# Kernel tuning notes

Hardware: AMD Instinct MI355X
Metric: run time of the kernel (lower is better)

Reference implementation:

```python
import jax, jax.numpy as jnp
import numpy as np

N_NODES = 50000
N_EDGES = 800000
DIM = 256
DEPTH = 4
N_REL = 4
EPS = 1e-5


def setup_inputs() -> dict:
    key = jax.random.key(0)
    ks = jax.random.split(key, 8)
    scale = 1.0 / np.sqrt(DIM)
    return {
        "node_embedding": jax.random.normal(ks[0], (N_NODES, DIM), jnp.float32),
        "weights": jax.random.normal(ks[1], (DEPTH, N_REL, DIM, DIM), jnp.float32) * scale,
        "roots": jax.random.normal(ks[2], (DEPTH, DIM, DIM), jnp.float32) * scale,
        "biases": jax.random.normal(ks[3], (DEPTH, DIM), jnp.float32) * 0.01,
        "ln_gamma": jnp.ones((DEPTH, DIM), jnp.float32),
        "ln_beta": jnp.zeros((DEPTH, DIM), jnp.float32),
        "edge_index": jax.random.randint(ks[4], (2, N_EDGES), 0, N_NODES, jnp.int32),
        "edge_type": jax.random.randint(ks[5], (N_EDGES,), 0, N_REL, jnp.int32),
    }


def _rgcn_layer(X, W, root, bias, gamma, beta, src, dst, etype, inv_deg):
    # RGCNConv with aggr='mean': per-relation transform, then per-relation mean
    # over incoming edges at the target node, summed across relations.
    h = jnp.einsum('ni,rio->rno', X, W)            # [R, N, D]
    msg = h[etype, src] * inv_deg[:, None]         # [E, D] gather + per-relation 1/deg
    agg = jax.ops.segment_sum(msg, dst, num_segments=X.shape[0])  # [N, D]
    out = agg + X @ root + bias
    # LayerNorm
    mu = jnp.mean(out, axis=-1, keepdims=True)
    var = jnp.mean(jnp.square(out - mu), axis=-1, keepdims=True)
    out = (out - mu) * jax.lax.rsqrt(var + EPS) * gamma + beta
    out = jax.nn.elu(out)
    return out + X  # residual connection (dropout p=0 -> identity)


def reference(node_embedding, weights, roots, biases, ln_gamma, ln_beta, edge_index, edge_type):
    src, dst = edge_index[0], edge_index[1]
    # per-(node, relation) in-degree for the relation-wise mean aggregation
    cnt = jnp.zeros((node_embedding.shape[0], N_REL), node_embedding.dtype)
    cnt = cnt.at[dst, edge_type].add(1.0)
    inv_deg = 1.0 / jnp.maximum(cnt[dst, edge_type], 1.0)  # [E]
    X = node_embedding
    for l in range(DEPTH):
        X = _rgcn_layer(X, weights[l], roots[l], biases[l], ln_gamma[l], ln_beta[l],
                        src, dst, edge_type, inv_deg)
    return X
```

## Files before the change

kernel.cpp:

```cpp
#include <hip/hip_runtime.h>
#include <hip/hip_bf16.h>
#include <stdint.h>

#define NN 50000
#define NE 800000
#define DD 256
#define NL 4
#define NRL 4
#define KT 1280
#define KA 1024

typedef float f32x4 __attribute__((ext_vector_type(4)));
typedef __bf16 bf16x8 __attribute__((ext_vector_type(8)));
typedef __bf16 bf16x4 __attribute__((ext_vector_type(4)));
typedef unsigned short u16x4 __attribute__((ext_vector_type(4)));

static __device__ __forceinline__ unsigned short f2bf(float f) {
  __bf16 h = (__bf16)f;
  return __builtin_bit_cast(unsigned short, h);
}

static __device__ __forceinline__ u16x4 pk4(f32x4 v) {
  u16x4 o;
  o.x = f2bf(v.x); o.y = f2bf(v.y); o.z = f2bf(v.z); o.w = f2bf(v.w);
  return o;
}

static __device__ __forceinline__ void async16(const void* g, void* l) {
  __builtin_amdgcn_global_load_lds(
      (const __attribute__((address_space(1))) unsigned int*)g,
      (__attribute__((address_space(3))) unsigned int*)l, 16, 0, 0);
}


__global__ __launch_bounds__(256) void k_hist(const int* __restrict__ ei,
                                              const int* __restrict__ et,
                                              int* __restrict__ cntNR) {
  int e = blockIdx.x * 256 + threadIdx.x;
  if (e >= NE) return;
  int dst = ei[NE + e];
  int r = et[e];
  atomicAdd(&cntNR[dst * 4 + r], 1);
}

__global__ __launch_bounds__(256) void k_scan1(const int* __restrict__ cntNR,
                                               int* __restrict__ offs,
                                               int* __restrict__ bsum) {
  __shared__ int sd[256];
  const int t = threadIdx.x;
  const int n = blockIdx.x * 256 + t;
  int deg = 0;
  if (n < NN) {
    const int* c = cntNR + n * 4;
    deg = c[0] + c[1] + c[2] + c[3];
  }
  sd[t] = deg;
  __syncthreads();
  int val = deg;
  for (int d = 1; d < 256; d <<= 1) {
    int other = (t >= d) ? sd[t - d] : 0;
    __syncthreads();
    val += other;
    sd[t] = val;
    __syncthreads();
  }
  if (n < NN) offs[n] = val - deg;
  if (t == 255) bsum[blockIdx.x] = val;
}

__global__ __launch_bounds__(256) void k_scan2(const int* __restrict__ bsum,
                                               int* __restrict__ boff, int nb) {
  __shared__ int sd[256];
  const int t = threadIdx.x;
  int v = (t < nb) ? bsum[t] : 0;
  sd[t] = v;
  __syncthreads();
  int val = v;
  for (int d = 1; d < 256; d <<= 1) {
    int other = (t >= d) ? sd[t - d] : 0;
    __syncthreads();
    val += other;
    sd[t] = val;
    __syncthreads();
  }
  boff[t] = val - v;
}

__global__ __launch_bounds__(256) void k_scan3(int* __restrict__ offs,
                                               const int* __restrict__ boff,
                                               int* __restrict__ cursor) {
  int n = blockIdx.x * 256 + threadIdx.x;
  if (n < NN) {
    int o = offs[n] + boff[blockIdx.x];
    offs[n] = o;
    cursor[n] = o;
  }
  if (n == 0) offs[NN] = NE;
}

__global__ __launch_bounds__(256) void k_scatter(const int* __restrict__ ei,
                                                 const int* __restrict__ et,
                                                 int* __restrict__ cursor,
                                                 uint32_t* __restrict__ packed) {
  int e = blockIdx.x * 256 + threadIdx.x;
  if (e >= NE) return;
  int src = ei[e];
  int dst = ei[NE + e];
  int r = et[e];
  int pos = atomicAdd(&cursor[dst], 1);
  packed[pos] = (uint32_t)src | ((uint32_t)r << 16);
}

__global__ __launch_bounds__(256) void k_wconv(const float* __restrict__ weights,
                                               const float* __restrict__ roots,
                                               __hip_bfloat16* __restrict__ WbigT) {
  int idx = blockIdx.x * 256 + threadIdx.x;
  if (idx >= NL * DD * KT) return;
  int l = idx / (DD * KT);
  int rem = idx - l * (DD * KT);
  int o = rem / KT;
  int k = rem - o * KT;
  float v;
  if (k < NRL * DD) {
    int r = k >> 8, i = k & 255;
    v = weights[(((size_t)(l * NRL + r) * DD) + i) * DD + o];
  } else {
    int i = k - NRL * DD;
    v = roots[((size_t)l * DD + i) * DD + o];
  }
  WbigT[idx] = __float2bfloat16(v);
}

__global__ __launch_bounds__(256) void k_cast(const float* __restrict__ X,
                                              __hip_bfloat16* __restrict__ Xbf) {
  int i = blockIdx.x * 256 + threadIdx.x;
  if (i >= NN * 64) return;
  const f32x4* Xv = (const f32x4*)X;
  ((u16x4*)Xbf)[i] = pk4(Xv[i]);
}


__global__ __launch_bounds__(256) void k_agg(const __hip_bfloat16* __restrict__ Xbf,
                                             const uint32_t* __restrict__ packed,
                                             const int* __restrict__ offs,
                                             const int* __restrict__ cntNR,
                                             __hip_bfloat16* __restrict__ Abig) {
  const int wid = (blockIdx.x * 256 + threadIdx.x) >> 6;
  const int lane = threadIdx.x & 63;
  if (wid >= NN) return;
  const int beg = offs[wid];
  const int end = offs[wid + 1];
  const bf16x4* __restrict__ Xv = (const bf16x4*)Xbf;

  f32x4 a0 = {0.f, 0.f, 0.f, 0.f}, a1 = a0, a2 = a0, a3 = a0;

  for (int e = beg; e < end; e += 8) {
    uint32_t pv[8];
    bf16x4 vv[8];
#pragma unroll
    for (int i = 0; i < 8; ++i) {
      int ee = e + i;
      ee = (ee < end) ? ee : (end - 1);
      pv[i] = packed[ee];
    }
#pragma unroll
    for (int i = 0; i < 8; ++i) {
      vv[i] = Xv[(int)(pv[i] & 0xFFFFu) * 64 + lane];
    }
    const int nv = end - e;
#pragma unroll
    for (int i = 0; i < 8; ++i) {
      if (i < nv) {
        int r = (int)(pv[i] >> 16);
        f32x4 v = {(float)vv[i][0], (float)vv[i][1], (float)vv[i][2], (float)vv[i][3]};
        if (r == 0) a0 += v;
        else if (r == 1) a1 += v;
        else if (r == 2) a2 += v;
        else a3 += v;
      }
    }
  }

  const int* c = cntNR + wid * 4;
  int c0 = c[0], c1 = c[1], c2 = c[2], c3 = c[3];
  float s0 = 1.0f / (float)(c0 > 1 ? c0 : 1);
  float s1 = 1.0f / (float)(c1 > 1 ? c1 : 1);
  float s2 = 1.0f / (float)(c2 > 1 ? c2 : 1);
  float s3 = 1.0f / (float)(c3 > 1 ? c3 : 1);

  u16x4* Arow = (u16x4*)(Abig + (size_t)wid * KA);
  Arow[0 * 64 + lane] = pk4(a0 * s0);
  Arow[1 * 64 + lane] = pk4(a1 * s1);
  Arow[2 * 64 + lane] = pk4(a2 * s2);
  Arow[3 * 64 + lane] = pk4(a3 * s3);
}


#define GBUF 20480
#define NTILE 40

__global__ __launch_bounds__(256, 2) void k_gemm(const __hip_bfloat16* __restrict__ A,
                                                 const __hip_bfloat16* __restrict__ Xbf_in,
                                                 const __hip_bfloat16* __restrict__ Bt,
                                                 const float* __restrict__ bias,
                                                 const float* __restrict__ gamma,
                                                 const float* __restrict__ beta,
                                                 const float* __restrict__ Xin,
                                                 float* __restrict__ Xout,
                                                 __hip_bfloat16* __restrict__ Xbf_out) {
  __shared__ __align__(16) char sLDS[4 * GBUF];
  float(*sRed)[4] = (float(*)[4])sLDS;

  const int tid = threadIdx.x;
  const int w = tid >> 6;
  const int lane = tid & 63;
  const int wm = w >> 1, wn = w & 1;
  const int quad = lane >> 4, l15 = lane & 15;
  const int mBase = blockIdx.x * 64;

  const int srow = lane >> 2;
  const int kc = (lane & 3) ^ ((srow >> 1) & 3);

  int am = mBase + w * 16 + srow;
  if (am >= NN) am = NN - 1;
  const char* agp = (const char*)A + (size_t)am * (KA * 2) + kc * 16;
  const char* agx = (const char*)Xbf_in + (size_t)am * (DD * 2) + kc * 16;
  const char* bgp0 = (const char*)Bt + (size_t)(w * 64 + 0 + srow) * (KT * 2) + kc * 16;
  const char* bgp1 = (const char*)Bt + (size_t)(w * 64 + 16 + srow) * (KT * 2) + kc * 16;
  const char* bgp2 = (const char*)Bt + (size_t)(w * 64 + 32 + srow) * (KT * 2) + kc * 16;
  const char* bgp3 = (const char*)Bt + (size_t)(w * 64 + 48 + srow) * (KT * 2) + kc * 16;

  char* const lA = sLDS + w * 1024;
  char* const lB = sLDS + 4096 + w * 4096;

  f32x4 acc[2][8];
#pragma unroll
  for (int i = 0; i < 2; ++i)
#pragma unroll
    for (int j = 0; j < 8; ++j) acc[i][j] = (f32x4){0.f, 0.f, 0.f, 0.f};

  const int aslot = (quad ^ ((l15 >> 1) & 3)) * 16;
  const char* const aBase = sLDS + (wm * 32 + l15) * 64 + aslot;
  const char* const bBase = sLDS + 4096 + (wn * 128 + l15) * 64 + aslot;

  auto STAGE = [&](int buf, int ts) {
    const int k0 = ts * 64;
    char* la = lA + buf * GBUF;
    char* lb = lB + buf * GBUF;
    if (k0 < KA * 2) {
      async16(agp + k0, la);
    } else {
      async16(agx + (k0 - KA * 2), la);
    }
    async16(bgp0 + k0, lb);
    async16(bgp1 + k0, lb + 1024);
    async16(bgp2 + k0, lb + 2048);
    async16(bgp3 + k0, lb + 3072);
  };

  auto COMPUTE = [&](int buf) {
    const char* aAddr = aBase + buf * GBUF;
    const char* bAddr = bBase + buf * GBUF;
    bf16x8 a0 = *(const bf16x8*)(aAddr + 0 * 1024);
    bf16x8 a1 = *(const bf16x8*)(aAddr + 1 * 1024);
#pragma unroll
    for (int nt = 0; nt < 8; ++nt) {
      bf16x8 b = *(const bf16x8*)(bAddr + nt * 1024);
      acc[0][nt] = __builtin_amdgcn_mfma_f32_16x16x32_bf16(a0, b, acc[0][nt], 0, 0, 0);
      acc[1][nt] = __builtin_amdgcn_mfma_f32_16x16x32_bf16(a1, b, acc[1][nt], 0, 0, 0);
    }
  };

  STAGE(0, 0);
  STAGE(1, 1);
  int cb = 0, sb = 2;
  for (int t = 0; t < NTILE - 2; ++t) {
    STAGE(sb, t + 2);
    __builtin_amdgcn_sched_barrier(0);
    asm volatile("s_waitcnt vmcnt(10)" ::: "memory");
    __builtin_amdgcn_s_barrier();
    __builtin_amdgcn_sched_barrier(0);
    COMPUTE(cb);
    cb = (cb + 1) & 3;
    sb = (sb + 1) & 3;
  }
  asm volatile("s_waitcnt vmcnt(5)" ::: "memory");
  __builtin_amdgcn_s_barrier();
  __builtin_amdgcn_sched_barrier(0);
  COMPUTE(cb);
  cb = (cb + 1) & 3;
  asm volatile("s_waitcnt vmcnt(0)" ::: "memory");
  __builtin_amdgcn_s_barrier();
  __builtin_amdgcn_sched_barrier(0);
  COMPUTE(cb);

  __syncthreads();

  float bv[8], gv[8], bev[8];
#pragma unroll
  for (int nt = 0; nt < 8; ++nt) {
    int n = wn * 128 + nt * 16 + l15;
    bv[nt] = bias[n];
    gv[nt] = gamma[n];
    bev[nt] = beta[n];
  }

#pragma unroll
  for (int mt = 0; mt < 2; ++mt) {
#pragma unroll
    for (int reg = 0; reg < 4; ++reg) {
      float s = 0.f, q = 0.f;
#pragma unroll
      for (int nt = 0; nt < 8; ++nt) {
        float v = acc[mt][nt][reg] + bv[nt];
        acc[mt][nt][reg] = v;
        s += v;
        q += v * v;
      }
#pragma unroll
      for (int d = 1; d < 16; d <<= 1) {
        s += __shfl_xor(s, d, 64);
        q += __shfl_xor(q, d, 64);
      }
      if (l15 == 0) {
        int row = wm * 32 + mt * 16 + quad * 4 + reg;
        sRed[row][wn * 2] = s;
        sRed[row][wn * 2 + 1] = q;
      }
    }
  }
  __syncthreads();

#pragma unroll
  for (int mt = 0; mt < 2; ++mt) {
#pragma unroll
    for (int reg = 0; reg < 4; ++reg) {
      int row = wm * 32 + mt * 16 + quad * 4 + reg;
      float ts = sRed[row][0] + sRed[row][2];
      float tq = sRed[row][1] + sRed[row][3];
      float mean = ts * (1.0f / 256.0f);
      float var = tq * (1.0f / 256.0f) - mean * mean;
      float rstd = rsqrtf(var + 1e-5f);
      int m = mBase + row;
      if (m < NN) {
#pragma unroll
        for (int nt = 0; nt < 8; ++nt) {
          int n = wn * 128 + nt * 16 + l15;
          float v = (acc[mt][nt][reg] - mean) * rstd * gv[nt] + bev[nt];
          v = v > 0.0f ? v : (__expf(v) - 1.0f);
          float res = v + __builtin_nontemporal_load(&Xin[(size_t)m * 256 + n]);
          __builtin_nontemporal_store(res, &Xout[(size_t)m * 256 + n]);
          Xbf_out[(size_t)m * 256 + n] = __float2bfloat16(res);
        }
      }
    }
  }
}


extern "C" void kernel_launch(void* const* d_in, const int* in_sizes, int n_in,
                              void* d_out, int out_size, void* d_ws, size_t ws_size,
                              hipStream_t stream) {
  const float* X0 = (const float*)d_in[0];
  const float* weights = (const float*)d_in[1];
  const float* roots = (const float*)d_in[2];
  const float* biases = (const float*)d_in[3];
  const float* ln_g = (const float*)d_in[4];
  const float* ln_b = (const float*)d_in[5];
  const int* eidx = (const int*)d_in[6];
  const int* etyp = (const int*)d_in[7];
  float* out = (float*)d_out;

  char* ws = (char*)d_ws;
  size_t off = 0;
  auto alloc = [&](size_t bytes) -> char* {
    char* p = ws + off;
    off = (off + bytes + 255) & ~(size_t)255;
    return p;
  };
  __hip_bfloat16* Abig = (__hip_bfloat16*)alloc((size_t)NN * KA * 2);
  __hip_bfloat16* WbigT = (__hip_bfloat16*)alloc((size_t)NL * DD * KT * 2);
  float* Xb0 = (float*)alloc((size_t)NN * DD * 4);
  float* Xb1 = (float*)alloc((size_t)NN * DD * 4);
  __hip_bfloat16* Xbf0 = (__hip_bfloat16*)alloc((size_t)NN * DD * 2);
  __hip_bfloat16* Xbf1 = (__hip_bfloat16*)alloc((size_t)NN * DD * 2);
  int* cntNR = (int*)alloc((size_t)NN * 4 * 4);
  int* offs = (int*)alloc((size_t)(NN + 1) * 4);
  int* cursor = (int*)alloc((size_t)NN * 4);
  uint32_t* packed = (uint32_t*)alloc((size_t)NE * 4);
  int* bsum = (int*)alloc(256 * 4);
  int* boff = (int*)alloc(256 * 4);
  (void)ws_size; (void)in_sizes; (void)n_in; (void)out_size;

  (void)hipMemsetAsync(cntNR, 0, (size_t)NN * 16, stream);
  k_hist<<<(NE + 255) / 256, 256, 0, stream>>>(eidx, etyp, cntNR);
  const int NB = (NN + 255) / 256;
  k_scan1<<<NB, 256, 0, stream>>>(cntNR, offs, bsum);
  k_scan2<<<1, 256, 0, stream>>>(bsum, boff, NB);
  k_scan3<<<NB, 256, 0, stream>>>(offs, boff, cursor);
  k_scatter<<<(NE + 255) / 256, 256, 0, stream>>>(eidx, etyp, cursor, packed);
  k_wconv<<<(NL * DD * KT + 255) / 256, 256, 0, stream>>>(weights, roots, WbigT);
  k_cast<<<(NN * 64 + 255) / 256, 256, 0, stream>>>(X0, Xbf0);

  const float* Xin = X0;
  for (int l = 0; l < NL; ++l) {
    float* Xout = (l == NL - 1) ? out : ((l & 1) ? Xb1 : Xb0);
    const __hip_bfloat16* Xbin = (l & 1) ? Xbf1 : Xbf0;
    __hip_bfloat16* Xbout = (l & 1) ? Xbf0 : Xbf1;
    k_agg<<<(NN * 64 + 255) / 256, 256, 0, stream>>>(Xbin, packed, offs, cntNR, Abig);
    k_gemm<<<(NN + 63) / 64, 256, 0, stream>>>(Abig, Xbin,
                                               WbigT + (size_t)l * DD * KT,
                                               biases + (size_t)l * DD,
                                               ln_g + (size_t)l * DD,
                                               ln_b + (size_t)l * DD, Xin, Xout, Xbout);
    Xin = Xout;
  }
}
```

Before: 866.4 us.

## Pre-tile and pre-swizzle aggregate and weight matrices into LDS-ready blocks

The aggregation kernel now writes its bf16 output in a tiled layout: per 64-row M-tile, per 32-wide K-slab, with the same XOR swizzle the GEMM uses in LDS. The weight conversion kernel emits the transposed weights in a matching K-slab-tiled, swizzled order. The GEMM's async loads then read contiguous 16-byte chunks per lane instead of strided row segments, which should make global loads fully coalesced. The cost is padding the aggregate buffer to whole tiles, plus an extra memset that zeroes the last partial tile.

```diff
diff --git a/kernel.cpp b/kernel.cpp
--- a/kernel.cpp
+++ b/kernel.cpp
@@ -9,6 +9,8 @@
 #define NRL 4
 #define KT 1280
 #define KA 1024
+#define NMT 782
+#define MTB 131072
 
 typedef float f32x4 __attribute__((ext_vector_type(4)));
 typedef __bf16 bf16x8 __attribute__((ext_vector_type(8)));
@@ -116,17 +118,21 @@
                                                __hip_bfloat16* __restrict__ WbigT) {
   int idx = blockIdx.x * 256 + threadIdx.x;
   if (idx >= NL * DD * KT) return;
-  int l = idx / (DD * KT);
-  int rem = idx - l * (DD * KT);
-  int o = rem / KT;
-  int k = rem - o * KT;
+  int l = idx / 327680;
+  int rem = idx - l * 327680;
+  int kt = rem / 8192;
+  int rem2 = rem - kt * 8192;
+  int row = rem2 >> 5;
+  int q = rem2 & 31;
+  int s = q >> 3, e = q & 7;
+  int k = kt * 32 + ((s ^ ((row >> 1) & 3)) << 3) + e;
   float v;
-  if (k < NRL * DD) {
+  if (k < KA) {
     int r = k >> 8, i = k & 255;
-    v = weights[(((size_t)(l * NRL + r) * DD) + i) * DD + o];
+    v = weights[(((size_t)(l * NRL + r) * DD) + i) * DD + row];
   } else {
-    int i = k - NRL * DD;
-    v = roots[((size_t)l * DD + i) * DD + o];
+    int i = k - KA;
+    v = roots[((size_t)l * DD + i) * DD + row];
   }
   WbigT[idx] = __float2bfloat16(v);
 }
@@ -188,11 +194,16 @@
   float s2 = 1.0f / (float)(c2 > 1 ? c2 : 1);
   float s3 = 1.0f / (float)(c3 > 1 ? c3 : 1);
 
-  u16x4* Arow = (u16x4*)(Abig + (size_t)wid * KA);
-  Arow[0 * 64 + lane] = pk4(a0 * s0);
-  Arow[1 * 64 + lane] = pk4(a1 * s1);
-  Arow[2 * 64 + lane] = pk4(a2 * s2);
-  Arow[3 * 64 + lane] = pk4(a3 * s3);
+  {
+    const int row = wid & 63;
+    const int fsw = (row >> 1) & 3;
+    char* Ab = (char*)Abig + (size_t)(wid >> 6) * MTB + (size_t)(lane >> 3) * 4096 +
+               row * 64 + ((((lane >> 1) & 3) ^ fsw) << 4) + (lane & 1) * 8;
+    *(u16x4*)(Ab + 0 * 32768) = pk4(a0 * s0);
+    *(u16x4*)(Ab + 1 * 32768) = pk4(a1 * s1);
+    *(u16x4*)(Ab + 2 * 32768) = pk4(a2 * s2);
+    *(u16x4*)(Ab + 3 * 32768) = pk4(a3 * s3);
+  }
 }
 
 
@@ -220,15 +231,12 @@
 
   const int srow = lane >> 2;
   const int kc = (lane & 3) ^ ((srow >> 1) & 3);
-
   int am = mBase + w * 16 + srow;
   if (am >= NN) am = NN - 1;
-  const char* agp = (const char*)A + (size_t)am * (KA * 2) + kc * 16;
   const char* agx = (const char*)Xbf_in + (size_t)am * (DD * 2) + kc * 16;
-  const char* bgp0 = (const char*)Bt + (size_t)(w * 64 + 0 + srow) * (KT * 2) + kc * 16;
-  const char* bgp1 = (const char*)Bt + (size_t)(w * 64 + 16 + srow) * (KT * 2) + kc * 16;
-  const char* bgp2 = (const char*)Bt + (size_t)(w * 64 + 32 + srow) * (KT * 2) + kc * 16;
-  const char* bgp3 = (const char*)Bt + (size_t)(w * 64 + 48 + srow) * (KT * 2) + kc * 16;
+
+  const char* agp = (const char*)A + (size_t)blockIdx.x * MTB + w * 1024 + lane * 16;
+  const char* bgp = (const char*)Bt + w * 4096 + lane * 16;
 
   char* const lA = sLDS + w * 1024;
   char* const lB = sLDS + 4096 + w * 4096;
@@ -244,18 +252,18 @@
   const char* const bBase = sLDS + 4096 + (wn * 128 + l15) * 64 + aslot;
 
   auto STAGE = [&](int buf, int ts) {
-    const int k0 = ts * 64;
     char* la = lA + buf * GBUF;
     char* lb = lB + buf * GBUF;
-    if (k0 < KA * 2) {
-      async16(agp + k0, la);
+    if (ts < 32) {
+      async16(agp + (size_t)ts * 4096, la);
     } else {
-      async16(agx + (k0 - KA * 2), la);
-    }
-    async16(bgp0 + k0, lb);
-    async16(bgp1 + k0, lb + 1024);
-    async16(bgp2 + k0, lb + 2048);
-    async16(bgp3 + k0, lb + 3072);
+      async16(agx + (ts - 32) * 64, la);
+    }
+    const char* bt = bgp + (size_t)ts * 16384;
+    async16(bt, lb);
+    async16(bt + 1024, lb + 1024);
+    async16(bt + 2048, lb + 2048);
+    async16(bt + 3072, lb + 3072);
   };
 
   auto COMPUTE = [&](int buf) {
@@ -378,7 +386,7 @@
     off = (off + bytes + 255) & ~(size_t)255;
     return p;
   };
-  __hip_bfloat16* Abig = (__hip_bfloat16*)alloc((size_t)NN * KA * 2);
+  __hip_bfloat16* Abig = (__hip_bfloat16*)alloc((size_t)NMT * MTB);
   __hip_bfloat16* WbigT = (__hip_bfloat16*)alloc((size_t)NL * DD * KT * 2);
   float* Xb0 = (float*)alloc((size_t)NN * DD * 4);
   float* Xb1 = (float*)alloc((size_t)NN * DD * 4);
@@ -393,6 +401,7 @@
   (void)ws_size; (void)in_sizes; (void)n_in; (void)out_size;
 
   (void)hipMemsetAsync(cntNR, 0, (size_t)NN * 16, stream);
+  (void)hipMemsetAsync((char*)Abig + (size_t)(NMT - 1) * MTB, 0, MTB, stream);
   k_hist<<<(NE + 255) / 256, 256, 0, stream>>>(eidx, etyp, cntNR);
   const int NB = (NN + 255) / 256;
   k_scan1<<<NB, 256, 0, stream>>>(cntNR, offs, bsum);
```

After: 800.5 us. -7.6%, faster.
